# Kernel optimization log

Hardware: AMD Instinct MI355X
Metric: run time of the kernel (lower is better)

## Reference

```python
import jax, jax.numpy as jnp
import numpy as np

B, C, H, W = 8, 48, 192, 192
N = H * W


def _bn_train(x, gamma, beta, eps=1e-5):
    # BatchNorm2d in training mode: biased batch stats over (B, H, W) per channel
    mean = jnp.mean(x, axis=(0, 2, 3), keepdims=True)
    var = jnp.var(x, axis=(0, 2, 3), keepdims=True)
    xn = (x - mean) * jax.lax.rsqrt(var + eps)
    return xn * gamma[None, :, None, None] + beta[None, :, None, None]


def _conv(x, w, b, pad):
    y = jax.lax.conv_general_dilated(
        x, w, window_strides=(1, 1), padding=[(pad, pad), (pad, pad)],
        dimension_numbers=('NCHW', 'OIHW', 'NCHW'))
    return y + b[None, :, None, None]


def setup_inputs() -> dict:
    key = jax.random.key(0)
    ks = jax.random.split(key, 16)
    s = 0.05
    inp = {
        'input_feature': jax.random.normal(ks[0], (B, C, H, W), jnp.float32),
        'fb': jax.random.normal(ks[1], (B, C, H, W), jnp.float32),
        'fc': jax.random.normal(ks[2], (B, C, H, W), jnp.float32),
        'fd': jax.random.normal(ks[3], (B, C, H, W), jnp.float32),
        'Wa': jax.random.normal(ks[4], (C, C), jnp.float32) * s,
        'Wb': jax.random.normal(ks[5], (C, C), jnp.float32) * s,
        'Wc': jax.random.normal(ks[6], (C, C), jnp.float32) * s,
        'Wd': jax.random.normal(ks[7], (C, C), jnp.float32) * s,
        'fuse_w': jax.random.normal(ks[8], (C, 4 * C, 1, 1), jnp.float32) * s,
        'fuse_b': jnp.zeros((C,), jnp.float32),
        'fuse_gamma': jnp.ones((C,), jnp.float32),
        'fuse_beta': jnp.zeros((C,), jnp.float32),
        'gamma_cam': jnp.full((1,), 0.5, jnp.float32),  # nn.Parameter (init 0; nonzero for testing)
        'out_w': jax.random.normal(ks[9], (C, C, 3, 3), jnp.float32) * s,
        'out_b': jnp.zeros((C,), jnp.float32),
        'out_gamma': jnp.ones((C,), jnp.float32),
        'out_beta': jnp.zeros((C,), jnp.float32),
    }
    return inp


def reference(input_feature, fb, fc, fd, Wa, Wb, Wc, Wd,
              fuse_w, fuse_b, fuse_gamma, fuse_beta, gamma_cam,
              out_w, out_b, out_gamma, out_beta):
    b, c, h, w = input_feature.shape
    n = h * w
    # Linear over channel dim: x.view(B,C,N).permute -> [B,N,C] @ W.T -> permute back = [B,C,N]
    def lin(x, Wm):
        return jnp.einsum('oc,bcn->bon', Wm, x.reshape(b, c, n))

    q = lin(input_feature, Wa)                      # [B,C,N] shared query
    K = jnp.stack([q, lin(fb, Wb), lin(fc, Wc), lin(fd, Wd)], axis=0)  # [4,B,C,N] (k==v)

    # Fused 4-branch channel attention: energy [4,B,C,C]
    energy = jnp.einsum('bcn,sbdn->sbcd', q, K)
    energy_new = jnp.max(energy, axis=-1, keepdims=True) - energy  # reversed softmax logits
    attention = jax.nn.softmax(energy_new, axis=-1)
    out4 = jnp.einsum('sbcd,sbdn->sbcn', attention, K)              # [4,B,C,N]

    # concat along channel dim in branch order -> [B,4C,H,W]
    cat = out4.transpose(1, 0, 2, 3).reshape(b, 4 * c, h, w)

    atten = jax.nn.relu(_bn_train(_conv(cat, fuse_w, fuse_b, pad=0), fuse_gamma, fuse_beta))
    out = gamma_cam[0] * atten + input_feature
    out = jax.nn.relu(_bn_train(_conv(out, out_w, out_b, pad=1), out_gamma, out_beta))
    return out
```

## Files before the change

kernel.cpp:

```cpp
#include <hip/hip_runtime.h>
#include <hip/hip_bf16.h>

#define C 48
#define C4 192
#define HW 192
#define NPIX (HW * HW)
#define BATCH 8
#define CNT (BATCH * NPIX)

#define APRE_OFF   0ull
#define G_OFF      14155776ull
#define STATS_OFF  14229504ull
#define M2_OFF     14229696ull
#define MIDT_BYTE  57213696ull
#define WB_BYTE    85525248ull

typedef __attribute__((ext_vector_type(8))) short short8;
typedef __attribute__((ext_vector_type(4))) float f32x4;

static __device__ __forceinline__ unsigned pkbf(float a, float b) {
    union { __hip_bfloat162 h; unsigned u; } t;
    t.h = __float22bfloat162_rn(make_float2(a, b));
    return t.u;
}
static __device__ __forceinline__ float lo2f(unsigned p) { return __uint_as_float(p << 16); }
static __device__ __forceinline__ float hi2f(unsigned p) { return __uint_as_float(p & 0xffff0000u); }
static __device__ __forceinline__ short f2bfs(float f) { return (short)(pkbf(f, f) & 0xffffu); }

__global__ __launch_bounds__(256) void k_gram_mfma(
    const float* __restrict__ x0, const float* __restrict__ x1,
    const float* __restrict__ x2, const float* __restrict__ x3,
    float* __restrict__ G)
{
    __shared__ short hibuf[C4 * 72];
    __shared__ short lobuf[C4 * 72];
    int b = blockIdx.y;
    int n0 = blockIdx.x * 512;
    int tid = threadIdx.x;
    int wid = tid >> 6, lane = tid & 63, col = lane & 15, quad = lane >> 4;

    const float* x0b = x0 + (size_t)b * C * NPIX;
    const float* x1b = x1 + (size_t)b * C * NPIX;
    const float* x2b = x2 + (size_t)b * C * NPIX;
    const float* x3b = x3 + (size_t)b * C * NPIX;

    f32x4 acc[3][3];
#pragma unroll
    for (int mt = 0; mt < 3; ++mt)
#pragma unroll
        for (int nt = 0; nt < 3; ++nt)
            acc[mt][nt] = (f32x4){0.f, 0.f, 0.f, 0.f};

    int scr = tid >> 4;
    int n4 = (tid & 15) * 4;

    for (int sub = 0; sub < 8; ++sub) {
        int nb = n0 + sub * 64;
        __syncthreads();
#pragma unroll
        for (int it = 0; it < 12; ++it) {
            int ch = scr + it * 16;
            int s = ch / C, c = ch - s * C;
            const float* xp = (s == 0) ? x0b : (s == 1) ? x1b : (s == 2) ? x2b : x3b;
            float4 v = *(const float4*)(xp + (size_t)c * NPIX + nb + n4);
            unsigned h01 = pkbf(v.x, v.y), h23 = pkbf(v.z, v.w);
            float r0 = v.x - lo2f(h01), r1 = v.y - hi2f(h01);
            float r2 = v.z - lo2f(h23), r3 = v.w - hi2f(h23);
            unsigned l01 = pkbf(r0, r1), l23 = pkbf(r2, r3);
            *(unsigned*)&hibuf[ch * 72 + n4]     = h01;
            *(unsigned*)&hibuf[ch * 72 + n4 + 2] = h23;
            *(unsigned*)&lobuf[ch * 72 + n4]     = l01;
            *(unsigned*)&lobuf[ch * 72 + n4 + 2] = l23;
        }
        __syncthreads();
#pragma unroll
        for (int kb = 0; kb < 2; ++kb) {
            int ko = kb * 32 + quad * 8;
            short8 ah[3], al[3], bh[3], bl[3];
#pragma unroll
            for (int mt = 0; mt < 3; ++mt) {
                ah[mt] = *(const short8*)&hibuf[(mt * 16 + col) * 72 + ko];
                al[mt] = *(const short8*)&lobuf[(mt * 16 + col) * 72 + ko];
            }
#pragma unroll
            for (int nt = 0; nt < 3; ++nt) {
                int row = (wid * 3 + nt) * 16 + col;
                bh[nt] = *(const short8*)&hibuf[row * 72 + ko];
                bl[nt] = *(const short8*)&lobuf[row * 72 + ko];
            }
#pragma unroll
            for (int mt = 0; mt < 3; ++mt)
#pragma unroll
                for (int nt = 0; nt < 3; ++nt) {
                    acc[mt][nt] = __builtin_amdgcn_mfma_f32_16x16x32_bf16(
                        ah[mt], bh[nt], acc[mt][nt], 0, 0, 0);
                    acc[mt][nt] = __builtin_amdgcn_mfma_f32_16x16x32_bf16(
                        ah[mt], bl[nt], acc[mt][nt], 0, 0, 0);
                    acc[mt][nt] = __builtin_amdgcn_mfma_f32_16x16x32_bf16(
                        al[mt], bh[nt], acc[mt][nt], 0, 0, 0);
                }
        }
    }
#pragma unroll
    for (int mt = 0; mt < 3; ++mt)
#pragma unroll
        for (int nt = 0; nt < 3; ++nt) {
            int g = (wid * 3 + nt) * 16 + col;
            int s = g / C, d = g - s * C;
#pragma unroll
            for (int j = 0; j < 4; ++j) {
                int c = mt * 16 + quad * 4 + j;
                atomicAdd(&G[(((size_t)s * BATCH + b) * C + c) * C + d],
                          acc[mt][nt][j]);
            }
        }
}

__global__ __launch_bounds__(256) void k_small(
    const float* __restrict__ G,
    const float* __restrict__ Wa, const float* __restrict__ Wb,
    const float* __restrict__ Wc, const float* __restrict__ Wd,
    const float* __restrict__ fuse_w, float* __restrict__ M2g)
{
    int s = blockIdx.x, b = blockIdx.y;
    const float* Ws = (s == 0) ? Wa : (s == 1) ? Wb : (s == 2) ? Wc : Wd;

    __shared__ float g[C * C], wsm[C * C], wam[C * C], fw[C * C];
    __shared__ float t[C * C], e[C * C], m[C * C];
    int tid = threadIdx.x;

    const float* Gb = G + ((size_t)s * BATCH + b) * C * C;
    for (int k = tid; k < C * C; k += 256) {
        g[k] = Gb[k];
        wsm[k] = Ws[k];
        wam[k] = Wa[k];
        int o = k / C, c = k % C;
        fw[k] = fuse_w[(size_t)o * C4 + s * C + c];
    }
    __syncthreads();

    for (int k = tid; k < C * C; k += 256) {
        int c = k / C, d = k % C;
        float a = 0.f;
        for (int q = 0; q < C; ++q) a += g[c * C + q] * wsm[d * C + q];
        t[k] = a;
    }
    __syncthreads();
    for (int k = tid; k < C * C; k += 256) {
        int c = k / C, d = k % C;
        float a = 0.f;
        for (int q = 0; q < C; ++q) a += wam[c * C + q] * t[q * C + d];
        e[k] = a;
    }
    __syncthreads();
    if (tid < C) {
        int c = tid;
        float mn = e[c * C];
        for (int d = 1; d < C; ++d) mn = fminf(mn, e[c * C + d]);
        float sum = 0.f;
        for (int d = 0; d < C; ++d) {
            float v = __expf(mn - e[c * C + d]);
            e[c * C + d] = v;
            sum += v;
        }
        float inv = 1.0f / sum;
        for (int d = 0; d < C; ++d) e[c * C + d] *= inv;
    }
    __syncthreads();
    for (int k = tid; k < C * C; k += 256) {
        int d = k / C, o = k % C;
        float a = 0.f;
        for (int q = 0; q < C; ++q) a += fw[o * C + q] * e[q * C + d];
        m[k] = a;
    }
    __syncthreads();
    float* out = M2g + ((size_t)b * 4 + s) * C * C;
    for (int k = tid; k < C * C; k += 256) {
        int c = k / C, o = k % C;
        float a = 0.f;
        for (int q = 0; q < C; ++q) a += wsm[q * C + c] * m[q * C + o];
        out[k] = a;
    }
}

static __device__ __forceinline__ unsigned ladr(unsigned row, unsigned x) {
    unsigned f = ((row >> 1) ^ (row >> 2)) & 7;
    return (row << 9) | (x ^ (f << 4));
}

__global__ __launch_bounds__(256) void k_apply_mfma(
    const float* __restrict__ x0, const float* __restrict__ x1,
    const float* __restrict__ x2, const float* __restrict__ x3,
    const float* __restrict__ M2g, const float* __restrict__ fuse_b,
    float* __restrict__ apre, float* __restrict__ stats)
{
    __shared__ __align__(16) char xbuf[64 * 512];
    __shared__ float sst[96];
    char* lb = xbuf;

    int b = blockIdx.y;
    int n0 = blockIdx.x * 256;
    int tid = threadIdx.x;
    int wid = tid >> 6, lane = tid & 63, col = lane & 15, quad = lane >> 4;

    const float* x0b = x0 + (size_t)b * C * NPIX;
    const float* x1b = x1 + (size_t)b * C * NPIX;
    const float* x2b = x2 + (size_t)b * C * NPIX;
    const float* x3b = x3 + (size_t)b * C * NPIX;

    if (tid < 96) sst[tid] = 0.f;

    const float* Mb = M2g + (size_t)b * 4 * C * C;
    for (int e = tid; e < 48 * 192; e += 256) {
        int k = e / 48, o = e - k * 48;
        *(short*)(lb + ladr(o, k * 2)) = f2bfs(Mb[(size_t)k * 48 + o]);
    }
    __syncthreads();

    short8 afr[3][6];
#pragma unroll
    for (int mt = 0; mt < 3; ++mt)
#pragma unroll
        for (int kq = 0; kq < 6; ++kq)
            afr[mt][kq] = *(const short8*)(lb + ladr(mt * 16 + col, kq * 64 + quad * 16));

    float fbv[3][4];
#pragma unroll
    for (int mt = 0; mt < 3; ++mt)
#pragma unroll
        for (int j = 0; j < 4; ++j)
            fbv[mt][j] = fuse_b[mt * 16 + quad * 4 + j];

    float s1[3][4] = {}, s2[3][4] = {};
    int nl = (wid << 4) + col;

    for (int sub = 0; sub < 4; ++sub) {
        int nb = n0 + sub * 64;
        __syncthreads();
#pragma unroll
        for (int it = 0; it < 6; ++it) {
            int ef = tid + it * 256;
            int p  = ef >> 4;
            int nq = (ef & 15) << 2;
            int s  = p / 24;
            int c2 = (p - s * 24) * 2;
            const float* xp = ((s == 0) ? x0b : (s == 1) ? x1b : (s == 2) ? x2b : x3b)
                              + (size_t)c2 * NPIX + nb + nq;
            float4 va = *(const float4*)xp;
            float4 vb = *(const float4*)(xp + NPIX);
            unsigned p4 = (unsigned)p * 4;
            *(unsigned*)(lb + ladr(nq + 0, p4)) = pkbf(va.x, vb.x);
            *(unsigned*)(lb + ladr(nq + 1, p4)) = pkbf(va.y, vb.y);
            *(unsigned*)(lb + ladr(nq + 2, p4)) = pkbf(va.z, vb.z);
            *(unsigned*)(lb + ladr(nq + 3, p4)) = pkbf(va.w, vb.w);
        }
        __syncthreads();

        f32x4 acc[3];
        acc[0] = (f32x4){0.f, 0.f, 0.f, 0.f};
        acc[1] = (f32x4){0.f, 0.f, 0.f, 0.f};
        acc[2] = (f32x4){0.f, 0.f, 0.f, 0.f};
#pragma unroll
        for (int kq = 0; kq < 6; ++kq) {
            short8 bfr = *(const short8*)(lb + ladr(nl, kq * 64 + quad * 16));
            acc[0] = __builtin_amdgcn_mfma_f32_16x16x32_bf16(afr[0][kq], bfr, acc[0], 0, 0, 0);
            acc[1] = __builtin_amdgcn_mfma_f32_16x16x32_bf16(afr[1][kq], bfr, acc[1], 0, 0, 0);
            acc[2] = __builtin_amdgcn_mfma_f32_16x16x32_bf16(afr[2][kq], bfr, acc[2], 0, 0, 0);
        }

        int n = nb + nl;
#pragma unroll
        for (int mt = 0; mt < 3; ++mt)
#pragma unroll
            for (int j = 0; j < 4; ++j) {
                int o = mt * 16 + quad * 4 + j;
                float val = acc[mt][j] + fbv[mt][j];
                apre[((size_t)b * C + o) * NPIX + n] = val;
                s1[mt][j] += val;
                s2[mt][j] += val * val;
            }
    }

#pragma unroll
    for (int mt = 0; mt < 3; ++mt)
#pragma unroll
        for (int j = 0; j < 4; ++j) {
            float a = s1[mt][j], q = s2[mt][j];
#pragma unroll
            for (int off = 8; off; off >>= 1) {
                a += __shfl_down(a, off, 16);
                q += __shfl_down(q, off, 16);
            }
            if (col == 0) {
                int o = mt * 16 + quad * 4 + j;
                atomicAdd(&sst[o], a);
                atomicAdd(&sst[48 + o], q);
            }
        }
    __syncthreads();
    if (tid < 96) atomicAdd(&stats[tid], sst[tid]);
}

__global__ __launch_bounds__(256) void k_bn1t(
    const float* __restrict__ apre, const float* __restrict__ inp,
    const float* __restrict__ stats, const float* __restrict__ gamma,
    const float* __restrict__ beta, const float* __restrict__ gcam,
    short* __restrict__ mid_t)
{
    __shared__ short t[64 * C];
    int b = blockIdx.y;
    int n0 = blockIdx.x * 64;
    int tid = threadIdx.x;
    const float invc = 1.0f / (float)CNT;
    float g = gcam[0];

#pragma unroll
    for (int it = 0; it < 3; ++it) {
        int e = tid + it * 256;
        int c = e >> 4, pq = (e & 15) * 4;
        float mu = stats[c] * invc;
        float var = stats[C + c] * invc - mu * mu;
        float sc = gamma[c] * rsqrtf(var + 1e-5f);
        float be = beta[c] - mu * sc;
        size_t base = ((size_t)b * C + c) * NPIX + n0 + pq;
        float4 v = *(const float4*)(apre + base);
        float4 x = *(const float4*)(inp + base);
        t[(pq + 0) * C + c] = f2bfs(fmaxf(v.x * sc + be, 0.f) * g + x.x);
        t[(pq + 1) * C + c] = f2bfs(fmaxf(v.y * sc + be, 0.f) * g + x.y);
        t[(pq + 2) * C + c] = f2bfs(fmaxf(v.z * sc + be, 0.f) * g + x.z);
        t[(pq + 3) * C + c] = f2bfs(fmaxf(v.w * sc + be, 0.f) * g + x.w);
    }
    __syncthreads();
    short* mb = mid_t + ((size_t)b * NPIX + n0) * C;
#pragma unroll
    for (int it = 0; it < 3; ++it) {
        int e = tid + it * 256;
        *(short4*)(mb + e * 4) = *(const short4*)&t[e * 4];
    }
}

__global__ __launch_bounds__(256) void k_prep(
    const float* __restrict__ outw, short* __restrict__ Wb)
{
    int idx = blockIdx.x * 256 + threadIdx.x;
    if (idx >= 9 * 48 * 64) return;
    int i = idx & 63;
    int o = (idx >> 6) % 48;
    int tap = idx / (64 * 48);
    float v = (i < C) ? outw[((size_t)o * C + i) * 9 + tap] : 0.f;
    Wb[idx] = f2bfs(v);
}

__global__ __launch_bounds__(256) void k_conv_mfma(
    const short* __restrict__ mid_t, const short* __restrict__ Wb,
    const float* __restrict__ bias, float* __restrict__ out,
    float* __restrict__ stats)
{
    __shared__ short xl[324 * 72];
    __shared__ float sst[96];
    int b = blockIdx.y;
    int ty = blockIdx.x / 12, tx = blockIdx.x % 12;
    int h0 = ty * 16, w0 = tx * 16;
    int tid = threadIdx.x;

    if (tid < 96) sst[tid] = 0.f;

    for (int ch = tid; ch < 2916; ch += 256) {
        int lpx = ch / 9, part = ch % 9;
        int hh = h0 - 1 + lpx / 18, ww = w0 - 1 + lpx % 18;
        short8 v = {0, 0, 0, 0, 0, 0, 0, 0};
        if (part < 6 && hh >= 0 && hh < HW && ww >= 0 && ww < HW)
            v = *(const short8*)(mid_t + ((size_t)b * NPIX + hh * HW + ww) * C + part * 8);
        *(short8*)(xl + lpx * 72 + part * 8) = v;
    }
    __syncthreads();

    int wid = tid >> 6, lane = tid & 63;
    int col = lane & 15, quad = lane >> 4;

    f32x4 acc[3][4];
#pragma unroll
    for (int mt = 0; mt < 3; ++mt)
#pragma unroll
        for (int rr = 0; rr < 4; ++rr)
            acc[mt][rr] = (f32x4){0.f, 0.f, 0.f, 0.f};

#pragma unroll
    for (int tap = 0; tap < 9; ++tap) {
        int dh = tap / 3, dw = tap % 3;
#pragma unroll
        for (int kb = 0; kb < 2; ++kb) {
            short8 afr[3];
#pragma unroll
            for (int mt = 0; mt < 3; ++mt)
                afr[mt] = *(const short8*)(Wb + ((size_t)(tap * 48 + mt * 16 + col)) * 64
                                               + kb * 32 + quad * 8);
#pragma unroll
            for (int rr = 0; rr < 4; ++rr) {
                int r = wid * 4 + rr;
                int lpx = (r + dh) * 18 + col + dw;
                short8 bfr = *(const short8*)(xl + lpx * 72 + kb * 32 + quad * 8);
#pragma unroll
                for (int mt = 0; mt < 3; ++mt)
                    acc[mt][rr] = __builtin_amdgcn_mfma_f32_16x16x32_bf16(
                        afr[mt], bfr, acc[mt][rr], 0, 0, 0);
            }
        }
    }

    float s1[3][4] = {}, s2[3][4] = {};
#pragma unroll
    for (int mt = 0; mt < 3; ++mt)
#pragma unroll
        for (int rr = 0; rr < 4; ++rr) {
            int r = wid * 4 + rr;
            f32x4 v = acc[mt][rr];
#pragma unroll
            for (int j = 0; j < 4; ++j) {
                int o = mt * 16 + quad * 4 + j;
                float val = v[j] + bias[o];
                out[((size_t)b * C + o) * NPIX + (h0 + r) * HW + w0 + col] = val;
                s1[mt][j] += val;
                s2[mt][j] += val * val;
            }
        }
#pragma unroll
    for (int mt = 0; mt < 3; ++mt)
#pragma unroll
        for (int j = 0; j < 4; ++j) {
            float a = s1[mt][j], q = s2[mt][j];
#pragma unroll
            for (int off = 8; off; off >>= 1) {
                a += __shfl_down(a, off, 16);
                q += __shfl_down(q, off, 16);
            }
            if (col == 0) {
                int o = mt * 16 + quad * 4 + j;
                atomicAdd(&sst[o], a);
                atomicAdd(&sst[48 + o], q);
            }
        }
    __syncthreads();
    if (tid < 48)       atomicAdd(&stats[2 * C + tid], sst[tid]);
    else if (tid < 96)  atomicAdd(&stats[3 * C + tid - 48], sst[tid]);
}

__global__ __launch_bounds__(256) void k_bn2(
    float* __restrict__ out, const float* __restrict__ stats,
    const float* __restrict__ gamma, const float* __restrict__ beta)
{
    size_t i = ((size_t)blockIdx.x * 256 + threadIdx.x) * 4;
    int c = (int)((i / NPIX) % C);
    const float invc = 1.0f / (float)CNT;
    float mu = stats[2 * C + c] * invc;
    float var = stats[3 * C + c] * invc - mu * mu;
    float sc = gamma[c] * rsqrtf(var + 1e-5f);
    float be = beta[c] - mu * sc;

    float4 v = *(float4*)(out + i);
    v.x = fmaxf(v.x * sc + be, 0.f);
    v.y = fmaxf(v.y * sc + be, 0.f);
    v.z = fmaxf(v.z * sc + be, 0.f);
    v.w = fmaxf(v.w * sc + be, 0.f);
    *(float4*)(out + i) = v;
}

extern "C" void kernel_launch(void* const* d_in, const int* in_sizes, int n_in,
                              void* d_out, int out_size, void* d_ws, size_t ws_size,
                              hipStream_t stream)
{
    const float* inp   = (const float*)d_in[0];
    const float* fb    = (const float*)d_in[1];
    const float* fc    = (const float*)d_in[2];
    const float* fd    = (const float*)d_in[3];
    const float* Wa    = (const float*)d_in[4];
    const float* Wbm   = (const float*)d_in[5];
    const float* Wcm   = (const float*)d_in[6];
    const float* Wdm   = (const float*)d_in[7];
    const float* fusew = (const float*)d_in[8];
    const float* fuseb = (const float*)d_in[9];
    const float* fgam  = (const float*)d_in[10];
    const float* fbet  = (const float*)d_in[11];
    const float* gcam  = (const float*)d_in[12];
    const float* outw  = (const float*)d_in[13];
    const float* outb  = (const float*)d_in[14];
    const float* ogam  = (const float*)d_in[15];
    const float* obet  = (const float*)d_in[16];

    float* ws    = (float*)d_ws;
    float* apre  = ws + APRE_OFF;
    float* G     = ws + G_OFF;
    float* stats = ws + STATS_OFF;
    float* M2g   = ws + M2_OFF;
    short* mid_t = (short*)((char*)d_ws + MIDT_BYTE);
    short* Wb    = (short*)((char*)d_ws + WB_BYTE);
    float* out   = (float*)d_out;

    hipMemsetAsync(G, 0, (73728ull + 192ull) * sizeof(float), stream);

    k_prep<<<108, 256, 0, stream>>>(outw, Wb);
    k_gram_mfma<<<dim3(72, BATCH), 256, 0, stream>>>(inp, fb, fc, fd, G);
    k_small<<<dim3(4, BATCH), 256, 0, stream>>>(G, Wa, Wbm, Wcm, Wdm, fusew, M2g);
    k_apply_mfma<<<dim3(144, BATCH), 256, 0, stream>>>(inp, fb, fc, fd, M2g, fuseb, apre, stats);
    k_bn1t<<<dim3(576, BATCH), 256, 0, stream>>>(apre, inp, stats, fgam, fbet, gcam, mid_t);
    k_conv_mfma<<<dim3(144, BATCH), 256, 0, stream>>>(mid_t, Wb, outb, out, stats);
    k_bn2<<<13824, 256, 0, stream>>>(out, stats, ogam, obet);
}
```

Before: 483.9 us.

## Software-pipeline gram kernel loads with register prefetch and double the grid

The gram kernel now prefetches the next two 64-pixel chunks into registers while the current chunk is packed and fed to MFMA, so global-load latency overlaps with compute. Each block now covers 256 pixels instead of 512, giving 144x8 blocks and twice as many atomic flushes into G. The LDS row pitch drops from 72 to 68 shorts, which changes the bank-conflict pattern, and launch bounds request 3 blocks per SM. The two prefetch buffers raise register pressure, which may cause spills under the occupancy hint.

```diff
diff --git a/kernel.cpp b/kernel.cpp
--- a/kernel.cpp
+++ b/kernel.cpp
@@ -27,15 +27,15 @@
 static __device__ __forceinline__ float hi2f(unsigned p) { return __uint_as_float(p & 0xffff0000u); }
 static __device__ __forceinline__ short f2bfs(float f) { return (short)(pkbf(f, f) & 0xffffu); }
 
-__global__ __launch_bounds__(256) void k_gram_mfma(
+__global__ __launch_bounds__(256, 3) void k_gram_mfma(
     const float* __restrict__ x0, const float* __restrict__ x1,
     const float* __restrict__ x2, const float* __restrict__ x3,
     float* __restrict__ G)
 {
-    __shared__ short hibuf[C4 * 72];
-    __shared__ short lobuf[C4 * 72];
+    __shared__ short hibuf[C4 * 68];
+    __shared__ short lobuf[C4 * 68];
     int b = blockIdx.y;
-    int n0 = blockIdx.x * 512;
+    int n0 = blockIdx.x * 256;
     int tid = threadIdx.x;
     int wid = tid >> 6, lane = tid & 63, col = lane & 15, quad = lane >> 4;
 
@@ -54,53 +54,78 @@
     int scr = tid >> 4;
     int n4 = (tid & 15) * 4;
 
-    for (int sub = 0; sub < 8; ++sub) {
-        int nb = n0 + sub * 64;
+#define GRAM_LOAD(dst, nb)                                                      \
+    _Pragma("unroll")                                                           \
+    for (int it = 0; it < 12; ++it) {                                           \
+        const float* xb = (it / 3 == 0) ? x0b : (it / 3 == 1) ? x1b             \
+                        : (it / 3 == 2) ? x2b : x3b;                            \
+        dst[it] = *(const float4*)(xb + (size_t)(scr + (it % 3) * 16) * NPIX    \
+                                      + (nb) + n4);                             \
+    }
+
+#define GRAM_PACK(src)                                                          \
+    _Pragma("unroll")                                                           \
+    for (int it = 0; it < 12; ++it) {                                           \
+        int ch = scr + it * 16;                                                 \
+        float4 v = src[it];                                                     \
+        unsigned h01 = pkbf(v.x, v.y), h23 = pkbf(v.z, v.w);                    \
+        float r0 = v.x - lo2f(h01), r1 = v.y - hi2f(h01);                       \
+        float r2 = v.z - lo2f(h23), r3 = v.w - hi2f(h23);                       \
+        unsigned l01 = pkbf(r0, r1), l23 = pkbf(r2, r3);                        \
+        *(uint2*)&hibuf[ch * 68 + n4] = make_uint2(h01, h23);                   \
+        *(uint2*)&lobuf[ch * 68 + n4] = make_uint2(l01, l23);                   \
+    }
+
+#define GRAM_MMA()                                                              \
+    _Pragma("unroll")                                                           \
+    for (int kb = 0; kb < 2; ++kb) {                                            \
+        int ko = kb * 32 + quad * 8;                                            \
+        short8 ah[3], al[3], bh[3], bl[3];                                      \
+        _Pragma("unroll")                                                       \
+        for (int mt = 0; mt < 3; ++mt) {                                        \
+            ah[mt] = *(const short8*)&hibuf[(mt * 16 + col) * 68 + ko];         \
+            al[mt] = *(const short8*)&lobuf[(mt * 16 + col) * 68 + ko];         \
+        }                                                                       \
+        _Pragma("unroll")                                                       \
+        for (int nt = 0; nt < 3; ++nt) {                                        \
+            int row = (wid * 3 + nt) * 16 + col;                                \
+            bh[nt] = *(const short8*)&hibuf[row * 68 + ko];                     \
+            bl[nt] = *(const short8*)&lobuf[row * 68 + ko];                     \
+        }                                                                       \
+        _Pragma("unroll")                                                       \
+        for (int mt = 0; mt < 3; ++mt)                                          \
+            _Pragma("unroll")                                                   \
+            for (int nt = 0; nt < 3; ++nt) {                                    \
+                acc[mt][nt] = __builtin_amdgcn_mfma_f32_16x16x32_bf16(          \
+                    ah[mt], bh[nt], acc[mt][nt], 0, 0, 0);                      \
+                acc[mt][nt] = __builtin_amdgcn_mfma_f32_16x16x32_bf16(          \
+                    ah[mt], bl[nt], acc[mt][nt], 0, 0, 0);                      \
+                acc[mt][nt] = __builtin_amdgcn_mfma_f32_16x16x32_bf16(          \
+                    al[mt], bh[nt], acc[mt][nt], 0, 0, 0);                      \
+            }                                                                   \
+    }
+
+    float4 preA[12], preB[12];
+    GRAM_LOAD(preA, n0)
+    GRAM_LOAD(preB, n0 + 64)
+
+#pragma unroll
+    for (int sp = 0; sp < 2; ++sp) {
+        GRAM_PACK(preA)
         __syncthreads();
-#pragma unroll
-        for (int it = 0; it < 12; ++it) {
-            int ch = scr + it * 16;
-            int s = ch / C, c = ch - s * C;
-            const float* xp = (s == 0) ? x0b : (s == 1) ? x1b : (s == 2) ? x2b : x3b;
-            float4 v = *(const float4*)(xp + (size_t)c * NPIX + nb + n4);
-            unsigned h01 = pkbf(v.x, v.y), h23 = pkbf(v.z, v.w);
-            float r0 = v.x - lo2f(h01), r1 = v.y - hi2f(h01);
-            float r2 = v.z - lo2f(h23), r3 = v.w - hi2f(h23);
-            unsigned l01 = pkbf(r0, r1), l23 = pkbf(r2, r3);
-            *(unsigned*)&hibuf[ch * 72 + n4]     = h01;
-            *(unsigned*)&hibuf[ch * 72 + n4 + 2] = h23;
-            *(unsigned*)&lobuf[ch * 72 + n4]     = l01;
-            *(unsigned*)&lobuf[ch * 72 + n4 + 2] = l23;
-        }
+        if (sp < 1) { GRAM_LOAD(preA, n0 + (2 * sp + 2) * 64) }
+        GRAM_MMA()
         __syncthreads();
-#pragma unroll
-        for (int kb = 0; kb < 2; ++kb) {
-            int ko = kb * 32 + quad * 8;
-            short8 ah[3], al[3], bh[3], bl[3];
-#pragma unroll
-            for (int mt = 0; mt < 3; ++mt) {
-                ah[mt] = *(const short8*)&hibuf[(mt * 16 + col) * 72 + ko];
-                al[mt] = *(const short8*)&lobuf[(mt * 16 + col) * 72 + ko];
-            }
-#pragma unroll
-            for (int nt = 0; nt < 3; ++nt) {
-                int row = (wid * 3 + nt) * 16 + col;
-                bh[nt] = *(const short8*)&hibuf[row * 72 + ko];
-                bl[nt] = *(const short8*)&lobuf[row * 72 + ko];
-            }
-#pragma unroll
-            for (int mt = 0; mt < 3; ++mt)
-#pragma unroll
-                for (int nt = 0; nt < 3; ++nt) {
-                    acc[mt][nt] = __builtin_amdgcn_mfma_f32_16x16x32_bf16(
-                        ah[mt], bh[nt], acc[mt][nt], 0, 0, 0);
-                    acc[mt][nt] = __builtin_amdgcn_mfma_f32_16x16x32_bf16(
-                        ah[mt], bl[nt], acc[mt][nt], 0, 0, 0);
-                    acc[mt][nt] = __builtin_amdgcn_mfma_f32_16x16x32_bf16(
-                        al[mt], bh[nt], acc[mt][nt], 0, 0, 0);
-                }
-        }
-    }
+        GRAM_PACK(preB)
+        __syncthreads();
+        if (sp < 1) { GRAM_LOAD(preB, n0 + (2 * sp + 3) * 64) }
+        GRAM_MMA()
+        __syncthreads();
+    }
+#undef GRAM_LOAD
+#undef GRAM_PACK
+#undef GRAM_MMA
+
 #pragma unroll
     for (int mt = 0; mt < 3; ++mt)
 #pragma unroll
@@ -499,7 +524,7 @@
     hipMemsetAsync(G, 0, (73728ull + 192ull) * sizeof(float), stream);
 
     k_prep<<<108, 256, 0, stream>>>(outw, Wb);
-    k_gram_mfma<<<dim3(72, BATCH), 256, 0, stream>>>(inp, fb, fc, fd, G);
+    k_gram_mfma<<<dim3(144, BATCH), 256, 0, stream>>>(inp, fb, fc, fd, G);
     k_small<<<dim3(4, BATCH), 256, 0, stream>>>(G, Wa, Wbm, Wcm, Wdm, fusew, M2g);
     k_apply_mfma<<<dim3(144, BATCH), 256, 0, stream>>>(inp, fb, fc, fd, M2g, fuseb, apre, stats);
     k_bn1t<<<dim3(576, BATCH), 256, 0, stream>>>(apre, inp, stats, fgam, fbet, gcam, mid_t);
```

After: 511.3 us. +5.7%, slower.
